# Optimization experiments

Hardware: AMD Instinct MI355X
Metric: run time of the kernel (lower is better)

Reference implementation:

```python
import jax, jax.numpy as jnp
import numpy as np
import math

NUM_REF = 8
STD = 5.0
B, D = 8192, 512


def setup_inputs() -> dict:
    key = jax.random.key(0)
    k1, k2 = jax.random.split(key)
    Struct = jax.random.normal(k1, (B, D), dtype=jnp.float32)
    Label = jax.random.uniform(k2, (B,), dtype=jnp.float32)
    return {"Struct": Struct, "Label": Label}


def reference(Struct, Label):
    # Pairwise |label_j - label_i| : [B, B]
    res_abs = jnp.abs(Label[None, :] - Label[:, None])
    # Num_ref nearest labels per sample (torch.sort ascending + take first K)
    _, idx = jax.lax.top_k(-res_abs, NUM_REF)          # [B, K]
    Struct_ref = Struct[idx]                            # [B, K, D]
    Label_ref = jax.lax.stop_gradient(Label[idx])       # [B, K] (detached)
    mean = Label[:, None]                               # [B, 1]
    # Gaussian smoothing weights, normalized over the K refs
    w = jnp.exp(-(Label_ref - mean) ** 2 / (2.0 * STD ** 2)) / (
        jnp.sqrt(jnp.asarray(2.0 * math.pi, Struct.dtype)) * STD)
    w = w / jnp.sum(w, axis=1, keepdims=True)           # [B, K]
    Struct_mean = jnp.einsum("bk,bkd->bd", w, Struct_ref)  # [B, D]
    # cosine similarity between Struct and Struct_mean, averaged over batch
    l1 = Struct / (1e-10 + jnp.linalg.norm(Struct, axis=1, keepdims=True))
    l2 = Struct_mean / (1e-10 + jnp.linalg.norm(Struct_mean, axis=1, keepdims=True))
    sim = jnp.mean(jnp.sum(l1 * l2, axis=1))
    return 1.0 - sim
```

## Files before the change

### kernel.cpp

```cpp
#include <hip/hip_runtime.h>
#include <math.h>

#define BN 8192
#define DN 512
#define KN 8
#define WIN 16

typedef unsigned long long u64;
typedef unsigned int u32;

#define OFF_K0    0
#define OFF_K1    65536
#define OFF_SIDX  131072
#define OFF_SLAB  163840
#define OFF_PART  196608

__device__ __forceinline__ u32 flip_f32(u32 f) {
  return f ^ (u32)(((int)f >> 31) | 0x80000000);
}

__device__ __forceinline__ u64 shfl_xor_u64(u64 v, int mask) {
  u32 lo = (u32)v, hi = (u32)(v >> 32);
  lo = (u32)__shfl_xor((int)lo, mask, 64);
  hi = (u32)__shfl_xor((int)hi, mask, 64);
  return ((u64)hi << 32) | lo;
}

__device__ __forceinline__ void lds_merge(const u64* in, u64* out, int R, int tid) {
  for (int o = tid; o < 1024; o += 512) {
    int off = o & (2 * R - 1);
    const u64* A = in + (o - off);
    const u64* B = A + R;
    int lo = off > R ? off - R : 0;
    int hi = off < R ? off : R;
    while (lo < hi) {
      int m = (lo + hi) >> 1;
      if (A[m] < B[off - m - 1]) lo = m + 1; else hi = m;
    }
    int a = lo, b = off - lo;
    u64 va = (a < R) ? A[a] : ~0ull;
    u64 vb = (b < R) ? B[b] : ~0ull;
    out[o] = va < vb ? va : vb;
  }
}

__global__ __launch_bounds__(512) void sort1_kernel(const float* __restrict__ L,
                                                    u64* __restrict__ keys) {
  __shared__ u64 bufA[1024];
  __shared__ u64 bufB[1024];
  const int tid  = threadIdx.x;
  const int lane = tid & 63;
  const int wv   = tid >> 6;
  const int base = blockIdx.x * 1024 + wv * 128;

  const int g0 = base + lane, g1 = base + 64 + lane;
  u64 v0 = ((u64)flip_f32(__float_as_uint(L[g0])) << 32) | (u32)g0;
  u64 v1 = ((u64)flip_f32(__float_as_uint(L[g1])) << 32) | (u32)g1;

#pragma unroll
  for (int k = 2; k <= 128; k <<= 1) {
#pragma unroll
    for (int j = 64; j > 0; j >>= 1) {
      if (j >= k) continue;
      if (j == 64) {
        u64 mn = v0 < v1 ? v0 : v1;
        u64 mx = v0 < v1 ? v1 : v0;
        v0 = mn; v1 = mx;
      } else {
        u64 o0 = shfl_xor_u64(v0, j);
        u64 o1 = shfl_xor_u64(v1, j);
        bool lower = (lane & j) == 0;
        bool up0, up1;
        if (k == 128)     { up0 = true;  up1 = true;  }
        else if (k == 64) { up0 = true;  up1 = false; }
        else { bool u = (lane & k) == 0; up0 = u; up1 = u; }
        bool t0 = (up0 == lower), t1 = (up1 == lower);
        v0 = t0 ? (v0 < o0 ? v0 : o0) : (v0 < o0 ? o0 : v0);
        v1 = t1 ? (v1 < o1 ? v1 : o1) : (v1 < o1 ? o1 : v1);
      }
    }
  }

  bufA[wv * 128 + lane]      = v0;
  bufA[wv * 128 + 64 + lane] = v1;
  __syncthreads();
  lds_merge(bufA, bufB, 128, tid); __syncthreads();
  lds_merge(bufB, bufA, 256, tid); __syncthreads();
  lds_merge(bufA, bufB, 512, tid); __syncthreads();

  keys[blockIdx.x * 1024 + tid]       = bufB[tid];
  keys[blockIdx.x * 1024 + 512 + tid] = bufB[512 + tid];
}

template <int RUN, bool FINAL>
__global__ __launch_bounds__(256) void merge_pass_kernel(const u64* __restrict__ in,
                                                         u64* __restrict__ outk,
                                                         int* __restrict__ sIdx,
                                                         float* __restrict__ sLab) {
  const int t = blockIdx.x * 256 + threadIdx.x;
  const int seg = t / (2 * RUN);
  const int o   = t & (2 * RUN - 1);
  const u64* A = in + seg * 2 * RUN;
  const u64* B = A + RUN;

  int lo = (o > RUN) ? (o - RUN) : 0;
  int hi = (o < RUN) ? o : RUN;
  while (lo < hi) {
    int a = (lo + hi) >> 1;
    if (A[a] < B[o - a - 1]) lo = a + 1; else hi = a;
  }
  const int a = lo, b = o - a;
  u64 va = (a < RUN) ? A[a] : ~0ull;
  u64 vb = (b < RUN) ? B[b] : ~0ull;
  u64 v = (va < vb) ? va : vb;

  if (FINAL) {
    u32 f = (u32)(v >> 32);
    u32 orig = (f & 0x80000000u) ? (f ^ 0x80000000u) : ~f;
    sIdx[t] = (int)(u32)v;
    sLab[t] = __uint_as_float(orig);
  } else {
    outk[t] = v;
  }
}

__global__ __launch_bounds__(256) void wmean_cos_kernel(const float* __restrict__ S,
                                                        const int* __restrict__ sortedIdx,
                                                        const float* __restrict__ sortedLab,
                                                        float* __restrict__ partials) {
  const int tid  = threadIdx.x;
  const int lane = tid & 63;
  const int wv   = tid >> 6;
  const int blk  = blockIdx.x;
  const int swz  = ((blk & 7) << 8) | (blk >> 3);
  const int p    = swz * 4 + wv;
  const int b    = sortedIdx[p];
  const float Lb = sortedLab[p];

  u64 key = ~0ull;
  {
    int q = p - WIN + lane;
    if (lane <= 2 * WIN && q >= 0 && q < BN) {
      float dist = fabsf(sortedLab[q] - Lb);
      key = ((u64)__float_as_uint(dist) << 32) | (u32)sortedIdx[q];
    }
  }
#pragma unroll
  for (int k = 2; k <= 64; k <<= 1) {
#pragma unroll
    for (int j = 32; j > 0; j >>= 1) {
      if (j >= k) continue;
      u64 o = shfl_xor_u64(key, j);
      bool lower = (lane & j) == 0;
      bool up = (k == 64) ? true : ((lane & k) == 0);
      key = (up == lower) ? (key < o ? key : o) : (key < o ? o : key);
    }
  }
  float e = 0.0f;
  if (lane < 8) {
    float d = __uint_as_float((u32)(key >> 32));
    e = expf(-d * d * (1.0f / 50.0f));
  }
  float ssum = e;
  ssum += __shfl_xor(ssum, 1, 64);
  ssum += __shfl_xor(ssum, 2, 64);
  ssum += __shfl_xor(ssum, 4, 64);
  float wn = e / ssum;

  int ix[KN]; float w[KN];
  int myidx = (int)(u32)key;
#pragma unroll
  for (int k = 0; k < KN; k++) {
    ix[k] = __shfl(myidx, k, 64);
    w[k]  = __shfl(wn,    k, 64);
  }

  const float4* Srow = (const float4*)(S + (size_t)b * DN);
  float4 s0 = Srow[lane];
  float4 s1 = Srow[lane + 64];

  float4 m0 = make_float4(0.f, 0.f, 0.f, 0.f);
  float4 m1 = make_float4(0.f, 0.f, 0.f, 0.f);
#pragma unroll
  for (int k = 0; k < KN; k++) {
    const float4* Nrow = (const float4*)(S + (size_t)ix[k] * DN);
    float4 n0 = Nrow[lane];
    float4 n1 = Nrow[lane + 64];
    float wk = w[k];
    m0.x = fmaf(wk, n0.x, m0.x); m0.y = fmaf(wk, n0.y, m0.y);
    m0.z = fmaf(wk, n0.z, m0.z); m0.w = fmaf(wk, n0.w, m0.w);
    m1.x = fmaf(wk, n1.x, m1.x); m1.y = fmaf(wk, n1.y, m1.y);
    m1.z = fmaf(wk, n1.z, m1.z); m1.w = fmaf(wk, n1.w, m1.w);
  }

  float dot = s0.x * m0.x + s0.y * m0.y + s0.z * m0.z + s0.w * m0.w
            + s1.x * m1.x + s1.y * m1.y + s1.z * m1.z + s1.w * m1.w;
  float ns  = s0.x * s0.x + s0.y * s0.y + s0.z * s0.z + s0.w * s0.w
            + s1.x * s1.x + s1.y * s1.y + s1.z * s1.z + s1.w * s1.w;
  float nm  = m0.x * m0.x + m0.y * m0.y + m0.z * m0.z + m0.w * m0.w
            + m1.x * m1.x + m1.y * m1.y + m1.z * m1.z + m1.w * m1.w;

#pragma unroll
  for (int off = 32; off > 0; off >>= 1) {
    dot += __shfl_down(dot, off, 64);
    ns  += __shfl_down(ns,  off, 64);
    nm  += __shfl_down(nm,  off, 64);
  }

  __shared__ float psim[4];
  if (lane == 0) {
    psim[wv] = dot / ((1e-10f + sqrtf(ns)) * (1e-10f + sqrtf(nm)));
  }
  __syncthreads();
  if (tid == 0) {
    partials[blk] = psim[0] + psim[1] + psim[2] + psim[3];
  }
}

__global__ __launch_bounds__(256) void finalize_kernel(const float* __restrict__ partials,
                                                       float* __restrict__ out) {
  const int tid = threadIdx.x;
  float s = 0.0f;
  for (int i = tid; i < 2048; i += 256) s += partials[i];
#pragma unroll
  for (int off = 32; off > 0; off >>= 1) s += __shfl_down(s, off, 64);
  __shared__ float ps[4];
  if ((tid & 63) == 0) ps[tid >> 6] = s;
  __syncthreads();
  if (tid == 0) {
    float tot = ps[0] + ps[1] + ps[2] + ps[3];
    out[0] = 1.0f - tot * (1.0f / (float)BN);
  }
}

extern "C" void kernel_launch(void* const* d_in, const int* in_sizes, int n_in,
                              void* d_out, int out_size, void* d_ws, size_t ws_size,
                              hipStream_t stream) {
  const float* S = (const float*)d_in[0];
  const float* L = (const float*)d_in[1];
  float* out = (float*)d_out;

  char* ws = (char*)d_ws;
  u64*   keys0     = (u64*)  (ws + OFF_K0);
  u64*   keys1     = (u64*)  (ws + OFF_K1);
  int*   sortedIdx = (int*)  (ws + OFF_SIDX);
  float* sortedLab = (float*)(ws + OFF_SLAB);
  float* partials  = (float*)(ws + OFF_PART);

  sort1_kernel<<<8, 512, 0, stream>>>(L, keys0);
  merge_pass_kernel<1024, false><<<32, 256, 0, stream>>>(keys0, keys1, nullptr, nullptr);
  merge_pass_kernel<2048, false><<<32, 256, 0, stream>>>(keys1, keys0, nullptr, nullptr);
  merge_pass_kernel<4096, true ><<<32, 256, 0, stream>>>(keys0, nullptr, sortedIdx, sortedLab);
  wmean_cos_kernel<<<2048, 256, 0, stream>>>(S, sortedIdx, sortedLab, partials);
  finalize_kernel <<<1, 256, 0, stream>>>(partials, out);
}
```

Measured before the change: 93.20 us.

## Fuse sort, merge passes, weighted-mean and reduction into one cooperative kernel

Replaces six separate launches with a single cooperative kernel of 256 blocks x 512 threads that uses grid.sync between the bitonic sort, the three merge passes, the weighted-mean cosine stage and the final reduction. Each wave now handles four samples in a loop instead of one, with the XCD-aware index swizzle kept. The aim is to remove per-launch overhead and gaps between the small, latency-bound sort/merge kernels. In exchange it adds grid-wide barrier costs and lowers parallelism in the gather stage, which may reduce latency hiding.

New measurement: 219.1 us. +135.1%, slower.

```diff
diff --git a/kernel.cpp b/kernel.cpp
--- a/kernel.cpp
+++ b/kernel.cpp
@@ -1,5 +1,8 @@
 #include <hip/hip_runtime.h>
+#include <hip/hip_cooperative_groups.h>
 #include <math.h>
+
+namespace cg = cooperative_groups;
 
 #define BN 8192
 #define DN 512
@@ -44,192 +47,214 @@
   }
 }
 
-__global__ __launch_bounds__(512) void sort1_kernel(const float* __restrict__ L,
-                                                    u64* __restrict__ keys) {
-  __shared__ u64 bufA[1024];
-  __shared__ u64 bufB[1024];
-  const int tid  = threadIdx.x;
-  const int lane = tid & 63;
-  const int wv   = tid >> 6;
-  const int base = blockIdx.x * 1024 + wv * 128;
-
-  const int g0 = base + lane, g1 = base + 64 + lane;
-  u64 v0 = ((u64)flip_f32(__float_as_uint(L[g0])) << 32) | (u32)g0;
-  u64 v1 = ((u64)flip_f32(__float_as_uint(L[g1])) << 32) | (u32)g1;
-
-#pragma unroll
-  for (int k = 2; k <= 128; k <<= 1) {
-#pragma unroll
-    for (int j = 64; j > 0; j >>= 1) {
-      if (j >= k) continue;
-      if (j == 64) {
-        u64 mn = v0 < v1 ? v0 : v1;
-        u64 mx = v0 < v1 ? v1 : v0;
-        v0 = mn; v1 = mx;
-      } else {
-        u64 o0 = shfl_xor_u64(v0, j);
-        u64 o1 = shfl_xor_u64(v1, j);
-        bool lower = (lane & j) == 0;
-        bool up0, up1;
-        if (k == 128)     { up0 = true;  up1 = true;  }
-        else if (k == 64) { up0 = true;  up1 = false; }
-        else { bool u = (lane & k) == 0; up0 = u; up1 = u; }
-        bool t0 = (up0 == lower), t1 = (up1 == lower);
-        v0 = t0 ? (v0 < o0 ? v0 : o0) : (v0 < o0 ? o0 : v0);
-        v1 = t1 ? (v1 < o1 ? v1 : o1) : (v1 < o1 ? o1 : v1);
-      }
-    }
-  }
-
-  bufA[wv * 128 + lane]      = v0;
-  bufA[wv * 128 + 64 + lane] = v1;
-  __syncthreads();
-  lds_merge(bufA, bufB, 128, tid); __syncthreads();
-  lds_merge(bufB, bufA, 256, tid); __syncthreads();
-  lds_merge(bufA, bufB, 512, tid); __syncthreads();
-
-  keys[blockIdx.x * 1024 + tid]       = bufB[tid];
-  keys[blockIdx.x * 1024 + 512 + tid] = bufB[512 + tid];
-}
-
 template <int RUN, bool FINAL>
-__global__ __launch_bounds__(256) void merge_pass_kernel(const u64* __restrict__ in,
-                                                         u64* __restrict__ outk,
-                                                         int* __restrict__ sIdx,
-                                                         float* __restrict__ sLab) {
-  const int t = blockIdx.x * 256 + threadIdx.x;
-  const int seg = t / (2 * RUN);
-  const int o   = t & (2 * RUN - 1);
-  const u64* A = in + seg * 2 * RUN;
-  const u64* B = A + RUN;
-
-  int lo = (o > RUN) ? (o - RUN) : 0;
-  int hi = (o < RUN) ? o : RUN;
-  while (lo < hi) {
-    int a = (lo + hi) >> 1;
-    if (A[a] < B[o - a - 1]) lo = a + 1; else hi = a;
-  }
-  const int a = lo, b = o - a;
-  u64 va = (a < RUN) ? A[a] : ~0ull;
-  u64 vb = (b < RUN) ? B[b] : ~0ull;
-  u64 v = (va < vb) ? va : vb;
-
-  if (FINAL) {
-    u32 f = (u32)(v >> 32);
-    u32 orig = (f & 0x80000000u) ? (f ^ 0x80000000u) : ~f;
-    sIdx[t] = (int)(u32)v;
-    sLab[t] = __uint_as_float(orig);
-  } else {
-    outk[t] = v;
-  }
-}
-
-__global__ __launch_bounds__(256) void wmean_cos_kernel(const float* __restrict__ S,
-                                                        const int* __restrict__ sortedIdx,
-                                                        const float* __restrict__ sortedLab,
-                                                        float* __restrict__ partials) {
+__device__ __forceinline__ void merge_device(const u64* __restrict__ in,
+                                             u64* __restrict__ outk,
+                                             int* __restrict__ sIdx,
+                                             float* __restrict__ sLab,
+                                             int t) {
+  if (t < BN) {
+    const int seg = t / (2 * RUN);
+    const int o   = t & (2 * RUN - 1);
+    const u64* A = in + seg * 2 * RUN;
+    const u64* B = A + RUN;
+
+    int lo = (o > RUN) ? (o - RUN) : 0;
+    int hi = (o < RUN) ? o : RUN;
+    while (lo < hi) {
+      int a = (lo + hi) >> 1;
+      if (A[a] < B[o - a - 1]) lo = a + 1; else hi = a;
+    }
+    const int a = lo, b = o - a;
+    u64 va = (a < RUN) ? A[a] : ~0ull;
+    u64 vb = (b < RUN) ? B[b] : ~0ull;
+    u64 v = (va < vb) ? va : vb;
+
+    if (FINAL) {
+      u32 f = (u32)(v >> 32);
+      u32 orig = (f & 0x80000000u) ? (f ^ 0x80000000u) : ~f;
+      sIdx[t] = (int)(u32)v;
+      sLab[t] = __uint_as_float(orig);
+    } else {
+      outk[t] = v;
+    }
+  }
+}
+
+__global__ __launch_bounds__(512, 2) void fused_kernel(const float* __restrict__ S,
+                                                       const float* __restrict__ L,
+                                                       u64* __restrict__ keys0,
+                                                       u64* __restrict__ keys1,
+                                                       int* __restrict__ sortedIdx,
+                                                       float* __restrict__ sortedLab,
+                                                       float* __restrict__ partials,
+                                                       float* __restrict__ out) {
+  cg::grid_group grid = cg::this_grid();
   const int tid  = threadIdx.x;
   const int lane = tid & 63;
   const int wv   = tid >> 6;
   const int blk  = blockIdx.x;
-  const int swz  = ((blk & 7) << 8) | (blk >> 3);
-  const int p    = swz * 4 + wv;
-  const int b    = sortedIdx[p];
-  const float Lb = sortedLab[p];
-
-  u64 key = ~0ull;
-  {
-    int q = p - WIN + lane;
-    if (lane <= 2 * WIN && q >= 0 && q < BN) {
-      float dist = fabsf(sortedLab[q] - Lb);
-      key = ((u64)__float_as_uint(dist) << 32) | (u32)sortedIdx[q];
-    }
-  }
-#pragma unroll
-  for (int k = 2; k <= 64; k <<= 1) {
-#pragma unroll
-    for (int j = 32; j > 0; j >>= 1) {
-      if (j >= k) continue;
-      u64 o = shfl_xor_u64(key, j);
-      bool lower = (lane & j) == 0;
-      bool up = (k == 64) ? true : ((lane & k) == 0);
-      key = (up == lower) ? (key < o ? key : o) : (key < o ? o : key);
-    }
-  }
-  float e = 0.0f;
-  if (lane < 8) {
-    float d = __uint_as_float((u32)(key >> 32));
-    e = expf(-d * d * (1.0f / 50.0f));
-  }
-  float ssum = e;
-  ssum += __shfl_xor(ssum, 1, 64);
-  ssum += __shfl_xor(ssum, 2, 64);
-  ssum += __shfl_xor(ssum, 4, 64);
-  float wn = e / ssum;
-
-  int ix[KN]; float w[KN];
-  int myidx = (int)(u32)key;
-#pragma unroll
-  for (int k = 0; k < KN; k++) {
-    ix[k] = __shfl(myidx, k, 64);
-    w[k]  = __shfl(wn,    k, 64);
-  }
-
-  const float4* Srow = (const float4*)(S + (size_t)b * DN);
-  float4 s0 = Srow[lane];
-  float4 s1 = Srow[lane + 64];
-
-  float4 m0 = make_float4(0.f, 0.f, 0.f, 0.f);
-  float4 m1 = make_float4(0.f, 0.f, 0.f, 0.f);
-#pragma unroll
-  for (int k = 0; k < KN; k++) {
-    const float4* Nrow = (const float4*)(S + (size_t)ix[k] * DN);
-    float4 n0 = Nrow[lane];
-    float4 n1 = Nrow[lane + 64];
-    float wk = w[k];
-    m0.x = fmaf(wk, n0.x, m0.x); m0.y = fmaf(wk, n0.y, m0.y);
-    m0.z = fmaf(wk, n0.z, m0.z); m0.w = fmaf(wk, n0.w, m0.w);
-    m1.x = fmaf(wk, n1.x, m1.x); m1.y = fmaf(wk, n1.y, m1.y);
-    m1.z = fmaf(wk, n1.z, m1.z); m1.w = fmaf(wk, n1.w, m1.w);
-  }
-
-  float dot = s0.x * m0.x + s0.y * m0.y + s0.z * m0.z + s0.w * m0.w
-            + s1.x * m1.x + s1.y * m1.y + s1.z * m1.z + s1.w * m1.w;
-  float ns  = s0.x * s0.x + s0.y * s0.y + s0.z * s0.z + s0.w * s0.w
-            + s1.x * s1.x + s1.y * s1.y + s1.z * s1.z + s1.w * s1.w;
-  float nm  = m0.x * m0.x + m0.y * m0.y + m0.z * m0.z + m0.w * m0.w
-            + m1.x * m1.x + m1.y * m1.y + m1.z * m1.z + m1.w * m1.w;
-
-#pragma unroll
-  for (int off = 32; off > 0; off >>= 1) {
-    dot += __shfl_down(dot, off, 64);
-    ns  += __shfl_down(ns,  off, 64);
-    nm  += __shfl_down(nm,  off, 64);
-  }
-
-  __shared__ float psim[4];
-  if (lane == 0) {
-    psim[wv] = dot / ((1e-10f + sqrtf(ns)) * (1e-10f + sqrtf(nm)));
-  }
+
+  __shared__ u64 bufA[1024];
+  __shared__ u64 bufB[1024];
+
+  if (blk < 8) {
+    const int base = blk * 1024 + wv * 128;
+    const int g0 = base + lane, g1 = base + 64 + lane;
+    u64 v0 = ((u64)flip_f32(__float_as_uint(L[g0])) << 32) | (u32)g0;
+    u64 v1 = ((u64)flip_f32(__float_as_uint(L[g1])) << 32) | (u32)g1;
+
+#pragma unroll
+    for (int k = 2; k <= 128; k <<= 1) {
+#pragma unroll
+      for (int j = 64; j > 0; j >>= 1) {
+        if (j >= k) continue;
+        if (j == 64) {
+          u64 mn = v0 < v1 ? v0 : v1;
+          u64 mx = v0 < v1 ? v1 : v0;
+          v0 = mn; v1 = mx;
+        } else {
+          u64 o0 = shfl_xor_u64(v0, j);
+          u64 o1 = shfl_xor_u64(v1, j);
+          bool lower = (lane & j) == 0;
+          bool up0, up1;
+          if (k == 128)     { up0 = true;  up1 = true;  }
+          else if (k == 64) { up0 = true;  up1 = false; }
+          else { bool u = (lane & k) == 0; up0 = u; up1 = u; }
+          bool t0 = (up0 == lower), t1 = (up1 == lower);
+          v0 = t0 ? (v0 < o0 ? v0 : o0) : (v0 < o0 ? o0 : v0);
+          v1 = t1 ? (v1 < o1 ? v1 : o1) : (v1 < o1 ? o1 : v1);
+        }
+      }
+    }
+
+    bufA[wv * 128 + lane]      = v0;
+    bufA[wv * 128 + 64 + lane] = v1;
+    __syncthreads();
+    lds_merge(bufA, bufB, 128, tid); __syncthreads();
+    lds_merge(bufB, bufA, 256, tid); __syncthreads();
+    lds_merge(bufA, bufB, 512, tid); __syncthreads();
+
+    keys0[blk * 1024 + tid]       = bufB[tid];
+    keys0[blk * 1024 + 512 + tid] = bufB[512 + tid];
+  }
+  grid.sync();
+
+  const int t = blk * 512 + tid;
+  merge_device<1024, false>(keys0, keys1, nullptr, nullptr, t);
+  grid.sync();
+  merge_device<2048, false>(keys1, keys0, nullptr, nullptr, t);
+  grid.sync();
+  merge_device<4096, true >(keys0, nullptr, sortedIdx, sortedLab, t);
+  grid.sync();
+
+  const int xcd  = blk & 7;
+  const int span = blk >> 3;
+  float wavesim = 0.0f;
+
+  for (int r = 0; r < 4; ++r) {
+    const int p  = xcd * 1024 + span * 32 + wv * 4 + r;
+    const int b  = sortedIdx[p];
+    const float Lb = sortedLab[p];
+
+    u64 key = ~0ull;
+    {
+      int q = p - WIN + lane;
+      if (lane <= 2 * WIN && q >= 0 && q < BN) {
+        float dist = fabsf(sortedLab[q] - Lb);
+        key = ((u64)__float_as_uint(dist) << 32) | (u32)sortedIdx[q];
+      }
+    }
+#pragma unroll
+    for (int k = 2; k <= 64; k <<= 1) {
+#pragma unroll
+      for (int j = 32; j > 0; j >>= 1) {
+        if (j >= k) continue;
+        u64 o = shfl_xor_u64(key, j);
+        bool lower = (lane & j) == 0;
+        bool up = (k == 64) ? true : ((lane & k) == 0);
+        key = (up == lower) ? (key < o ? key : o) : (key < o ? o : key);
+      }
+    }
+    float e = 0.0f;
+    if (lane < 8) {
+      float d = __uint_as_float((u32)(key >> 32));
+      e = expf(-d * d * (1.0f / 50.0f));
+    }
+    float ssum = e;
+    ssum += __shfl_xor(ssum, 1, 64);
+    ssum += __shfl_xor(ssum, 2, 64);
+    ssum += __shfl_xor(ssum, 4, 64);
+    float wn = e / ssum;
+
+    int ix[KN]; float w[KN];
+    int myidx = (int)(u32)key;
+#pragma unroll
+    for (int k = 0; k < KN; k++) {
+      ix[k] = __shfl(myidx, k, 64);
+      w[k]  = __shfl(wn,    k, 64);
+    }
+
+    const float4* Srow = (const float4*)(S + (size_t)b * DN);
+    float4 s0 = Srow[lane];
+    float4 s1 = Srow[lane + 64];
+
+    float4 m0 = make_float4(0.f, 0.f, 0.f, 0.f);
+    float4 m1 = make_float4(0.f, 0.f, 0.f, 0.f);
+#pragma unroll
+    for (int k = 0; k < KN; k++) {
+      const float4* Nrow = (const float4*)(S + (size_t)ix[k] * DN);
+      float4 n0 = Nrow[lane];
+      float4 n1 = Nrow[lane + 64];
+      float wk = w[k];
+      m0.x = fmaf(wk, n0.x, m0.x); m0.y = fmaf(wk, n0.y, m0.y);
+      m0.z = fmaf(wk, n0.z, m0.z); m0.w = fmaf(wk, n0.w, m0.w);
+      m1.x = fmaf(wk, n1.x, m1.x); m1.y = fmaf(wk, n1.y, m1.y);
+      m1.z = fmaf(wk, n1.z, m1.z); m1.w = fmaf(wk, n1.w, m1.w);
+    }
+
+    float dot = s0.x * m0.x + s0.y * m0.y + s0.z * m0.z + s0.w * m0.w
+              + s1.x * m1.x + s1.y * m1.y + s1.z * m1.z + s1.w * m1.w;
+    float ns  = s0.x * s0.x + s0.y * s0.y + s0.z * s0.z + s0.w * s0.w
+              + s1.x * s1.x + s1.y * s1.y + s1.z * s1.z + s1.w * s1.w;
+    float nm  = m0.x * m0.x + m0.y * m0.y + m0.z * m0.z + m0.w * m0.w
+              + m1.x * m1.x + m1.y * m1.y + m1.z * m1.z + m1.w * m1.w;
+
+#pragma unroll
+    for (int off = 32; off > 0; off >>= 1) {
+      dot += __shfl_down(dot, off, 64);
+      ns  += __shfl_down(ns,  off, 64);
+      nm  += __shfl_down(nm,  off, 64);
+    }
+    if (lane == 0) {
+      wavesim += dot / ((1e-10f + sqrtf(ns)) * (1e-10f + sqrtf(nm)));
+    }
+  }
+
+  __shared__ float psim[8];
+  if (lane == 0) psim[wv] = wavesim;
   __syncthreads();
   if (tid == 0) {
-    partials[blk] = psim[0] + psim[1] + psim[2] + psim[3];
-  }
-}
-
-__global__ __launch_bounds__(256) void finalize_kernel(const float* __restrict__ partials,
-                                                       float* __restrict__ out) {
-  const int tid = threadIdx.x;
-  float s = 0.0f;
-  for (int i = tid; i < 2048; i += 256) s += partials[i];
-#pragma unroll
-  for (int off = 32; off > 0; off >>= 1) s += __shfl_down(s, off, 64);
-  __shared__ float ps[4];
-  if ((tid & 63) == 0) ps[tid >> 6] = s;
-  __syncthreads();
-  if (tid == 0) {
-    float tot = ps[0] + ps[1] + ps[2] + ps[3];
-    out[0] = 1.0f - tot * (1.0f / (float)BN);
+    float s = 0.0f;
+#pragma unroll
+    for (int i = 0; i < 8; i++) s += psim[i];
+    partials[blk] = s;
+  }
+  grid.sync();
+
+  if (blk == 0) {
+    float s = (tid < 256) ? partials[tid] : 0.0f;
+#pragma unroll
+    for (int off = 32; off > 0; off >>= 1) s += __shfl_down(s, off, 64);
+    __shared__ float ps[8];
+    if (lane == 0) ps[wv] = s;
+    __syncthreads();
+    if (tid == 0) {
+      float tot = 0.0f;
+#pragma unroll
+      for (int i = 0; i < 8; i++) tot += ps[i];
+      out[0] = 1.0f - tot * (1.0f / (float)BN);
+    }
   }
 }
 
@@ -247,10 +272,9 @@
   float* sortedLab = (float*)(ws + OFF_SLAB);
   float* partials  = (float*)(ws + OFF_PART);
 
-  sort1_kernel<<<8, 512, 0, stream>>>(L, keys0);
-  merge_pass_kernel<1024, false><<<32, 256, 0, stream>>>(keys0, keys1, nullptr, nullptr);
-  merge_pass_kernel<2048, false><<<32, 256, 0, stream>>>(keys1, keys0, nullptr, nullptr);
-  merge_pass_kernel<4096, true ><<<32, 256, 0, stream>>>(keys0, nullptr, sortedIdx, sortedLab);
-  wmean_cos_kernel<<<2048, 256, 0, stream>>>(S, sortedIdx, sortedLab, partials);
-  finalize_kernel <<<1, 256, 0, stream>>>(partials, out);
-}
+  void* args[] = { (void*)&S, (void*)&L, (void*)&keys0, (void*)&keys1,
+                   (void*)&sortedIdx, (void*)&sortedLab, (void*)&partials,
+                   (void*)&out };
+  hipLaunchCooperativeKernel((const void*)fused_kernel, dim3(256), dim3(512),
+                             args, 0, stream);
+}
```

## Fuse final merge pass into weighted-mean kernel and process 16 rows per block

Applied to the files above, without the earlier changes.

Removes the last global merge-pass launch. Each wmean block now recomputes its 48-key window of the final sorted order by running a merge-path binary search over the two 4096-element runs and stores it in shared memory. Each wave then handles 4 consecutive sorted rows in a loop, so the grid shrinks from 2048 to 512 blocks and finalize sums 512 partials. This saves one kernel launch and the sortedIdx/sortedLab round trip, at the cost of redundant binary searches and less parallelism per launch.

Result: no change. 93.65 us (+0.5%).

```diff
diff --git a/kernel.cpp b/kernel.cpp
--- a/kernel.cpp
+++ b/kernel.cpp
@@ -11,12 +11,13 @@
 
 #define OFF_K0    0
 #define OFF_K1    65536
-#define OFF_SIDX  131072
-#define OFF_SLAB  163840
-#define OFF_PART  196608
+#define OFF_PART  131072
 
 __device__ __forceinline__ u32 flip_f32(u32 f) {
   return f ^ (u32)(((int)f >> 31) | 0x80000000);
+}
+__device__ __forceinline__ float unflip_f32(u32 f) {
+  return __uint_as_float((f & 0x80000000u) ? (f ^ 0x80000000u) : ~f);
 }
 
 __device__ __forceinline__ u64 shfl_xor_u64(u64 v, int mask) {
@@ -92,11 +93,9 @@
   keys[blockIdx.x * 1024 + 512 + tid] = bufB[512 + tid];
 }
 
-template <int RUN, bool FINAL>
+template <int RUN>
 __global__ __launch_bounds__(256) void merge_pass_kernel(const u64* __restrict__ in,
-                                                         u64* __restrict__ outk,
-                                                         int* __restrict__ sIdx,
-                                                         float* __restrict__ sLab) {
+                                                         u64* __restrict__ outk) {
   const int t = blockIdx.x * 256 + threadIdx.x;
   const int seg = t / (2 * RUN);
   const int o   = t & (2 * RUN - 1);
@@ -112,105 +111,128 @@
   const int a = lo, b = o - a;
   u64 va = (a < RUN) ? A[a] : ~0ull;
   u64 vb = (b < RUN) ? B[b] : ~0ull;
-  u64 v = (va < vb) ? va : vb;
-
-  if (FINAL) {
-    u32 f = (u32)(v >> 32);
-    u32 orig = (f & 0x80000000u) ? (f ^ 0x80000000u) : ~f;
-    sIdx[t] = (int)(u32)v;
-    sLab[t] = __uint_as_float(orig);
-  } else {
-    outk[t] = v;
-  }
+  outk[t] = (va < vb) ? va : vb;
 }
 
 __global__ __launch_bounds__(256) void wmean_cos_kernel(const float* __restrict__ S,
-                                                        const int* __restrict__ sortedIdx,
-                                                        const float* __restrict__ sortedLab,
+                                                        const u64* __restrict__ keys,
                                                         float* __restrict__ partials) {
   const int tid  = threadIdx.x;
   const int lane = tid & 63;
   const int wv   = tid >> 6;
   const int blk  = blockIdx.x;
-  const int swz  = ((blk & 7) << 8) | (blk >> 3);
-  const int p    = swz * 4 + wv;
-  const int b    = sortedIdx[p];
-  const float Lb = sortedLab[p];
-
-  u64 key = ~0ull;
-  {
-    int q = p - WIN + lane;
-    if (lane <= 2 * WIN && q >= 0 && q < BN) {
-      float dist = fabsf(sortedLab[q] - Lb);
-      key = ((u64)__float_as_uint(dist) << 32) | (u32)sortedIdx[q];
-    }
-  }
-#pragma unroll
-  for (int k = 2; k <= 64; k <<= 1) {
-#pragma unroll
-    for (int j = 32; j > 0; j >>= 1) {
-      if (j >= k) continue;
-      u64 o = shfl_xor_u64(key, j);
-      bool lower = (lane & j) == 0;
-      bool up = (k == 64) ? true : ((lane & k) == 0);
-      key = (up == lower) ? (key < o ? key : o) : (key < o ? o : key);
-    }
-  }
-  float e = 0.0f;
-  if (lane < 8) {
-    float d = __uint_as_float((u32)(key >> 32));
-    e = expf(-d * d * (1.0f / 50.0f));
-  }
-  float ssum = e;
-  ssum += __shfl_xor(ssum, 1, 64);
-  ssum += __shfl_xor(ssum, 2, 64);
-  ssum += __shfl_xor(ssum, 4, 64);
-  float wn = e / ssum;
-
-  int ix[KN]; float w[KN];
-  int myidx = (int)(u32)key;
-#pragma unroll
-  for (int k = 0; k < KN; k++) {
-    ix[k] = __shfl(myidx, k, 64);
-    w[k]  = __shfl(wn,    k, 64);
-  }
-
-  const float4* Srow = (const float4*)(S + (size_t)b * DN);
-  float4 s0 = Srow[lane];
-  float4 s1 = Srow[lane + 64];
-
-  float4 m0 = make_float4(0.f, 0.f, 0.f, 0.f);
-  float4 m1 = make_float4(0.f, 0.f, 0.f, 0.f);
-#pragma unroll
-  for (int k = 0; k < KN; k++) {
-    const float4* Nrow = (const float4*)(S + (size_t)ix[k] * DN);
-    float4 n0 = Nrow[lane];
-    float4 n1 = Nrow[lane + 64];
-    float wk = w[k];
-    m0.x = fmaf(wk, n0.x, m0.x); m0.y = fmaf(wk, n0.y, m0.y);
-    m0.z = fmaf(wk, n0.z, m0.z); m0.w = fmaf(wk, n0.w, m0.w);
-    m1.x = fmaf(wk, n1.x, m1.x); m1.y = fmaf(wk, n1.y, m1.y);
-    m1.z = fmaf(wk, n1.z, m1.z); m1.w = fmaf(wk, n1.w, m1.w);
-  }
-
-  float dot = s0.x * m0.x + s0.y * m0.y + s0.z * m0.z + s0.w * m0.w
-            + s1.x * m1.x + s1.y * m1.y + s1.z * m1.z + s1.w * m1.w;
-  float ns  = s0.x * s0.x + s0.y * s0.y + s0.z * s0.z + s0.w * s0.w
-            + s1.x * s1.x + s1.y * s1.y + s1.z * s1.z + s1.w * s1.w;
-  float nm  = m0.x * m0.x + m0.y * m0.y + m0.z * m0.z + m0.w * m0.w
-            + m1.x * m1.x + m1.y * m1.y + m1.z * m1.z + m1.w * m1.w;
-
-#pragma unroll
-  for (int off = 32; off > 0; off >>= 1) {
-    dot += __shfl_down(dot, off, 64);
-    ns  += __shfl_down(ns,  off, 64);
-    nm  += __shfl_down(nm,  off, 64);
+  const int xcd  = blk & 7;
+  const int span = blk >> 3;
+  const int base = xcd * 1024 + span * 16;
+
+  __shared__ u64 win[48];
+
+  if (tid < 48) {
+    int q = base - WIN + tid;
+    u64 v = ~0ull;
+    if (q >= 0 && q < BN) {
+      const u64* A = keys;
+      const u64* B = keys + 4096;
+      int lo = (q > 4096) ? (q - 4096) : 0;
+      int hi = (q < 4096) ? q : 4096;
+      while (lo < hi) {
+        int a = (lo + hi) >> 1;
+        if (A[a] < B[q - a - 1]) lo = a + 1; else hi = a;
+      }
+      int a = lo, b = q - lo;
+      u64 va = (a < 4096) ? A[a] : ~0ull;
+      u64 vb = (b < 4096) ? B[b] : ~0ull;
+      v = (va < vb) ? va : vb;
+    }
+    win[tid] = v;
+  }
+  __syncthreads();
+
+  float wavesim = 0.0f;
+
+  for (int r = 0; r < 4; ++r) {
+    const int rw = wv * 4 + r;
+    const u64 ckey = win[rw + WIN];
+    const float Lb = unflip_f32((u32)(ckey >> 32));
+    const int   b  = (int)(u32)ckey;
+
+    u64 key = ~0ull;
+    if (lane <= 2 * WIN) {
+      u64 k = win[rw + lane];
+      if (k != ~0ull) {
+        float lab = unflip_f32((u32)(k >> 32));
+        float dist = fabsf(lab - Lb);
+        key = ((u64)__float_as_uint(dist) << 32) | (u32)k;
+      }
+    }
+#pragma unroll
+    for (int k = 2; k <= 64; k <<= 1) {
+#pragma unroll
+      for (int j = 32; j > 0; j >>= 1) {
+        if (j >= k) continue;
+        u64 o = shfl_xor_u64(key, j);
+        bool lower = (lane & j) == 0;
+        bool up = (k == 64) ? true : ((lane & k) == 0);
+        key = (up == lower) ? (key < o ? key : o) : (key < o ? o : key);
+      }
+    }
+    float e = 0.0f;
+    if (lane < 8) {
+      float d = __uint_as_float((u32)(key >> 32));
+      e = expf(-d * d * (1.0f / 50.0f));
+    }
+    float ssum = e;
+    ssum += __shfl_xor(ssum, 1, 64);
+    ssum += __shfl_xor(ssum, 2, 64);
+    ssum += __shfl_xor(ssum, 4, 64);
+    float wn = e / ssum;
+
+    int ix[KN]; float w[KN];
+    int myidx = (int)(u32)key;
+#pragma unroll
+    for (int k = 0; k < KN; k++) {
+      ix[k] = __shfl(myidx, k, 64);
+      w[k]  = __shfl(wn,    k, 64);
+    }
+
+    const float4* Srow = (const float4*)(S + (size_t)b * DN);
+    float4 s0 = Srow[lane];
+    float4 s1 = Srow[lane + 64];
+
+    float4 m0 = make_float4(0.f, 0.f, 0.f, 0.f);
+    float4 m1 = make_float4(0.f, 0.f, 0.f, 0.f);
+#pragma unroll
+    for (int k = 0; k < KN; k++) {
+      const float4* Nrow = (const float4*)(S + (size_t)ix[k] * DN);
+      float4 n0 = Nrow[lane];
+      float4 n1 = Nrow[lane + 64];
+      float wk = w[k];
+      m0.x = fmaf(wk, n0.x, m0.x); m0.y = fmaf(wk, n0.y, m0.y);
+      m0.z = fmaf(wk, n0.z, m0.z); m0.w = fmaf(wk, n0.w, m0.w);
+      m1.x = fmaf(wk, n1.x, m1.x); m1.y = fmaf(wk, n1.y, m1.y);
+      m1.z = fmaf(wk, n1.z, m1.z); m1.w = fmaf(wk, n1.w, m1.w);
+    }
+
+    float dot = s0.x * m0.x + s0.y * m0.y + s0.z * m0.z + s0.w * m0.w
+              + s1.x * m1.x + s1.y * m1.y + s1.z * m1.z + s1.w * m1.w;
+    float ns  = s0.x * s0.x + s0.y * s0.y + s0.z * s0.z + s0.w * s0.w
+              + s1.x * s1.x + s1.y * s1.y + s1.z * s1.z + s1.w * s1.w;
+    float nm  = m0.x * m0.x + m0.y * m0.y + m0.z * m0.z + m0.w * m0.w
+              + m1.x * m1.x + m1.y * m1.y + m1.z * m1.z + m1.w * m1.w;
+
+#pragma unroll
+    for (int off = 32; off > 0; off >>= 1) {
+      dot += __shfl_down(dot, off, 64);
+      ns  += __shfl_down(ns,  off, 64);
+      nm  += __shfl_down(nm,  off, 64);
+    }
+    if (lane == 0) {
+      wavesim += dot / ((1e-10f + sqrtf(ns)) * (1e-10f + sqrtf(nm)));
+    }
   }
 
   __shared__ float psim[4];
-  if (lane == 0) {
-    psim[wv] = dot / ((1e-10f + sqrtf(ns)) * (1e-10f + sqrtf(nm)));
-  }
+  if (lane == 0) psim[wv] = wavesim;
   __syncthreads();
   if (tid == 0) {
     partials[blk] = psim[0] + psim[1] + psim[2] + psim[3];
@@ -221,7 +243,7 @@
                                                        float* __restrict__ out) {
   const int tid = threadIdx.x;
   float s = 0.0f;
-  for (int i = tid; i < 2048; i += 256) s += partials[i];
+  for (int i = tid; i < 512; i += 256) s += partials[i];
 #pragma unroll
   for (int off = 32; off > 0; off >>= 1) s += __shfl_down(s, off, 64);
   __shared__ float ps[4];
@@ -241,16 +263,13 @@
   float* out = (float*)d_out;
 
   char* ws = (char*)d_ws;
-  u64*   keys0     = (u64*)  (ws + OFF_K0);
-  u64*   keys1     = (u64*)  (ws + OFF_K1);
-  int*   sortedIdx = (int*)  (ws + OFF_SIDX);
-  float* sortedLab = (float*)(ws + OFF_SLAB);
-  float* partials  = (float*)(ws + OFF_PART);
+  u64*   keys0    = (u64*)  (ws + OFF_K0);
+  u64*   keys1    = (u64*)  (ws + OFF_K1);
+  float* partials = (float*)(ws + OFF_PART);
 
   sort1_kernel<<<8, 512, 0, stream>>>(L, keys0);
-  merge_pass_kernel<1024, false><<<32, 256, 0, stream>>>(keys0, keys1, nullptr, nullptr);
-  merge_pass_kernel<2048, false><<<32, 256, 0, stream>>>(keys1, keys0, nullptr, nullptr);
-  merge_pass_kernel<4096, true ><<<32, 256, 0, stream>>>(keys0, nullptr, sortedIdx, sortedLab);
-  wmean_cos_kernel<<<2048, 256, 0, stream>>>(S, sortedIdx, sortedLab, partials);
+  merge_pass_kernel<1024><<<32, 256, 0, stream>>>(keys0, keys1);
+  merge_pass_kernel<2048><<<32, 256, 0, stream>>>(keys1, keys0);
+  wmean_cos_kernel<<<512, 256, 0, stream>>>(S, keys0, partials);
   finalize_kernel <<<1, 256, 0, stream>>>(partials, out);
 }
```
